# Performance work log

Measured on AMD Instinct MI355X. Metric: run time of the kernel, lower is better.

## Reference

```python
import jax, jax.numpy as jnp
import numpy as np

N = 128          # n_nodes (hardcoded groups=128 in the torch module)
TIME_DIM = 16
XYZ_DIM = 63
SIGMA = 0.3
EPS = 0.01
relu = jax.nn.relu


def gconv(x, W, b):
    # grouped 1x1 Conv1d with groups=N: per-node GEMM
    # x: (N, Cin, L), W: (N, Cout, Cin), b: (N, Cout) -> (N, Cout, L)
    return jnp.einsum('ncl,nkc->nkl', x, W) + b[:, :, None]


def setup_inputs() -> dict:
    key = jax.random.key(0)
    ks = iter(jax.random.split(key, 64))

    def W(shape, fan_in):
        return jax.random.normal(next(ks), shape, jnp.float32) / np.float32(np.sqrt(fan_in))

    def bvec(shape):
        return 0.01 * jax.random.normal(next(ks), shape, jnp.float32)

    B, V = 1, 2048
    inp = {
        'poses': 0.1 * jax.random.normal(next(ks), (B, N, 24, 3), jnp.float32),
        't_ped': jax.random.normal(next(ks), (B, TIME_DIM), jnp.float32),
        'w': jax.random.uniform(next(ks), (N, 24), jnp.float32),
        'wpts': jax.random.uniform(next(ks), (B, V, 3), jnp.float32),
        'nodes_posed': jax.random.uniform(next(ks), (B, N, 3), jnp.float32),
        'local_coords': jax.random.normal(next(ks), (N, B, V, XYZ_DIM), jnp.float32),
        # encoder grouped convs
        'Wec1': W((N, 64, 72 + TIME_DIM), 72 + TIME_DIM), 'bec1': bvec((N, 64)),
        'Wec21': W((N, 8, 64), 64), 'bec21': bvec((N, 8)),
        'Wec22': W((N, 8, 64), 64), 'bec22': bvec((N, 8)),
        # decoder grouped convs
        'Wdc1': W((N, 64, 80), 80), 'bdc1': bvec((N, 64)),
        'Wdc21': W((N, 32, 64), 64), 'bdc21': bvec((N, 32)),
        'Wdc22': W((N, 3, 64), 64), 'bdc22': bvec((N, 3)),
        # feature-field grouped convs
        'Wf1': W((N, 64, 32 + XYZ_DIM), 32 + XYZ_DIM), 'bf1': bvec((N, 64)),
        'Wf2': W((N, 64, 64), 64), 'bf2': bvec((N, 64)),
        'Wf3': W((N, 64, 64), 64), 'bf3': bvec((N, 64)),
        'Wf4': W((N, 256, 64), 64), 'bf4': bvec((N, 256)),
        # Nerf head linears
        'Wc1': W((256, 64), 256), 'bc1': bvec((64,)),
        'Wc2': W((64, 3), 64), 'bc2': bvec((3,)),
        'Wd1': W((256, 1), 256), 'bd1': bvec((1,)),
    }
    return inp


def reference(poses, t_ped, w, wpts, nodes_posed, local_coords,
              Wec1, bec1, Wec21, bec21, Wec22, bec22,
              Wdc1, bdc1, Wdc21, bdc21, Wdc22, bdc22,
              Wf1, bf1, Wf2, bf2, Wf3, bf3, Wf4, bf4,
              Wc1, bc1, Wc2, bc2, Wd1, bd1):
    B, V = poses.shape[0], wpts.shape[1]

    # attention-weighted poses: (B, N, 72)
    poses_w = (w[None, :, :, None] * poses).reshape(B, N, 72)

    # ---- encode ----
    t = jnp.broadcast_to(t_ped[:, None, :], (B, N, TIME_DIM))
    enc_in = jnp.concatenate([poses_w, t], axis=-1).transpose(1, 2, 0)   # (N, 72+td, B)
    net = relu(gconv(enc_in, Wec1, bec1))                                # (N, 64, B)
    mean = gconv(net, Wec21, bec21).transpose(0, 2, 1)                   # (N, B, 8)
    logvar = gconv(net, Wec22, bec22).transpose(0, 2, 1)                 # (N, B, 8)
    z = mean  # eval-mode reparameterize

    # ---- decode ----
    dec_in = jnp.concatenate([poses_w, z.transpose(1, 0, 2)], axis=-1).transpose(1, 2, 0)  # (N, 80, B)
    net = relu(gconv(dec_in, Wdc1, bdc1))
    ei = gconv(net, Wdc21, bdc21).transpose(0, 2, 1)                     # (N, B, 32)
    delta_ni = gconv(net, Wdc22, bdc22).transpose(0, 2, 1)               # (N, B, 3)

    # ---- blend weights: RBF influence of each node on each point ----
    diff = wpts[None, :, :, :] - nodes_posed.transpose(1, 0, 2)[:, :, None, :]  # (N, B, V, 3)
    d2 = jnp.sum(diff * diff, axis=-1)                                   # (N, B, V)
    influ = jnp.exp(-d2 / (2.0 * SIGMA * SIGMA)) - EPS
    mask = influ >= 0
    bweights = jnp.maximum(influ, 0.0)

    # ---- feature field (dense per-node MLP, masked; == padded gather/scatter) ----
    raw = jnp.concatenate([jnp.broadcast_to(ei[:, :, None, :], (N, B, V, 32)),
                           local_coords], axis=-1)                       # (N, B, V, 32+xyz)
    x = raw.reshape(N, B * V, 32 + XYZ_DIM).transpose(0, 2, 1)           # (N, Cin, B*V)
    net = relu(gconv(x, Wf1, bf1))
    net = relu(gconv(net, Wf2, bf2))
    net = relu(gconv(net, Wf3, bf3))
    fout = relu(gconv(net, Wf4, bf4))                                    # (N, 256, B*V)
    f = fout.transpose(0, 2, 1).reshape(N, B, V, 256) * mask[..., None].astype(fout.dtype)

    # ---- blend features ----
    bw = bweights.transpose(1, 2, 0) + 1e-7                              # (B, V, N)
    bw = bw / jnp.sum(bw, axis=-1, keepdims=True)
    f_blend = jnp.einsum('nbvc,bvn->bvc', f, bw)                         # (B, V, 256)

    # ---- Nerf head ----
    netc = relu(f_blend @ Wc1 + bc1)
    c = netc @ Wc2 + bc2                                                 # (B, V, 3)
    d = relu(f_blend @ Wd1 + bd1)                                        # (B, V, 1)
    return (c, d, ei, delta_ni, mean, logvar)
```

## Files before the change

### kernel.cpp

```cpp
#include <hip/hip_runtime.h>

typedef __bf16 bf16;
typedef __bf16 bf16x4 __attribute__((ext_vector_type(4)));
typedef float  f32x4  __attribute__((ext_vector_type(4)));

#define NPTS 2048
#define XS_LD 68
#define W1_LD 100

__global__ __launch_bounds__(256) void k_sniff(const void* poses_raw, int* flag)
{
    __shared__ int cnt;
    if (threadIdx.x == 0) cnt = 0;
    __syncthreads();
    const bf16* pb = (const bf16*)poses_raw;
    int local = 0;
    for (int i = threadIdx.x; i < 9216; i += 256) {
        float v = (float)pb[i];
        if (!(v >= -2.0f && v <= 2.0f)) local++;
    }
    atomicAdd(&cnt, local);
    __syncthreads();
    if (threadIdx.x == 0) *flag = (cnt < 64) ? 1 : 0;
}

template<typename T, int WANT>
__global__ __launch_bounds__(128) void k_encdec_t(
    const T* __restrict__ poses, const T* __restrict__ t_ped, const T* __restrict__ w,
    const T* __restrict__ Wec1, const T* __restrict__ bec1,
    const T* __restrict__ Wec21, const T* __restrict__ bec21,
    const T* __restrict__ Wec22, const T* __restrict__ bec22,
    const T* __restrict__ Wdc1, const T* __restrict__ bdc1,
    const T* __restrict__ Wdc21, const T* __restrict__ bdc21,
    const T* __restrict__ Wdc22, const T* __restrict__ bdc22,
    T* __restrict__ out_ei, T* __restrict__ out_delta,
    T* __restrict__ out_mean, T* __restrict__ out_logvar,
    const int* __restrict__ flag)
{
    if (*flag != WANT) return;
    int n = blockIdx.x, tid = threadIdx.x;
    __shared__ float sin_[88], zbuf[8], net1[64], din[80], net2[64];
    if (tid < 72)      sin_[tid] = (float)w[n*24 + tid/3] * (float)poses[n*72 + tid];
    else if (tid < 88) sin_[tid] = (float)t_ped[tid - 72];
    __syncthreads();
    if (tid < 64) {
        float a = (float)bec1[n*64 + tid];
        const T* wr = Wec1 + (size_t)(n*64 + tid) * 88;
        for (int c = 0; c < 88; ++c) a += (float)wr[c] * sin_[c];
        net1[tid] = fmaxf(a, 0.f);
    }
    __syncthreads();
    if (tid < 8) {
        float a = (float)bec21[n*8 + tid];
        const T* wr = Wec21 + (size_t)(n*8 + tid) * 64;
        for (int c = 0; c < 64; ++c) a += (float)wr[c] * net1[c];
        out_mean[n*8 + tid] = (T)a;
        zbuf[tid] = a;
    } else if (tid < 16) {
        int o = tid - 8;
        float a = (float)bec22[n*8 + o];
        const T* wr = Wec22 + (size_t)(n*8 + o) * 64;
        for (int c = 0; c < 64; ++c) a += (float)wr[c] * net1[c];
        out_logvar[n*8 + o] = (T)a;
    }
    __syncthreads();
    if (tid < 72)      din[tid] = sin_[tid];
    else if (tid < 80) din[tid] = zbuf[tid - 72];
    __syncthreads();
    if (tid < 64) {
        float a = (float)bdc1[n*64 + tid];
        const T* wr = Wdc1 + (size_t)(n*64 + tid) * 80;
        for (int c = 0; c < 80; ++c) a += (float)wr[c] * din[c];
        net2[tid] = fmaxf(a, 0.f);
    }
    __syncthreads();
    if (tid < 32) {
        float a = (float)bdc21[n*32 + tid];
        const T* wr = Wdc21 + (size_t)(n*32 + tid) * 64;
        for (int c = 0; c < 64; ++c) a += (float)wr[c] * net2[c];
        out_ei[n*32 + tid] = (T)a;
    } else if (tid < 35) {
        int o = tid - 32;
        float a = (float)bdc22[n*3 + o];
        const T* wr = Wdc22 + (size_t)(n*3 + o) * 64;
        for (int c = 0; c < 64; ++c) a += (float)wr[c] * net2[c];
        out_delta[n*3 + o] = (T)a;
    }
}

template<typename T, int WANT>
__global__ __launch_bounds__(256) void k_bweights_t(
    const T* __restrict__ wpts, const T* __restrict__ nodes,
    float* __restrict__ wgt, const int* __restrict__ flag)
{
    if (*flag != WANT) return;
    int v = blockIdx.x * 256 + threadIdx.x;
    float px = (float)wpts[v*3+0], py = (float)wpts[v*3+1], pz = (float)wpts[v*3+2];
    float denom = 0.f;
    for (int n = 0; n < 128; ++n) {
        float dx = px - (float)nodes[n*3+0];
        float dy = py - (float)nodes[n*3+1];
        float dz = pz - (float)nodes[n*3+2];
        float d2 = dx*dx + dy*dy + dz*dz;
        float influ = expf(-d2 * (1.0f/0.18f)) - 0.01f;
        denom += fmaxf(influ, 0.f) + 1e-7f;
    }
    float inv = 1.f / denom;
    for (int n = 0; n < 128; ++n) {
        float dx = px - (float)nodes[n*3+0];
        float dy = py - (float)nodes[n*3+1];
        float dz = pz - (float)nodes[n*3+2];
        float d2 = dx*dx + dy*dy + dz*dz;
        float influ = expf(-d2 * (1.0f/0.18f)) - 0.01f;
        wgt[n*NPTS + v] = (influ >= 0.f) ? (fmaxf(influ, 0.f) + 1e-7f) * inv : 0.f;
    }
}


__device__ __forceinline__ f32x4 loadw4(const float* p) { return *(const f32x4*)p; }
__device__ __forceinline__ f32x4 loadw4(const bf16* p)
{
    bf16x4 v = *(const bf16x4*)p;
    f32x4 r;
    #pragma unroll
    for (int j = 0; j < 4; ++j) r[j] = (float)v[j];
    return r;
}

template<typename T>
__device__ __forceinline__ void layer64(
    const T* __restrict__ Wbase, const T* __restrict__ bbase,
    const float* __restrict__ hin, float* __restrict__ hout,
    int og, int pg)
{
    float acc[4][4] = {};
    #pragma unroll 4
    for (int k0 = 0; k0 < 64; k0 += 4) {
        f32x4 wv[4], xv[4];
        #pragma unroll
        for (int c = 0; c < 4; ++c) wv[c] = loadw4(Wbase + (size_t)(og*4 + c)*64 + k0);
        #pragma unroll
        for (int j = 0; j < 4; ++j) xv[j] = *(const f32x4*)&hin[(k0 + j)*XS_LD + pg*4];
        #pragma unroll
        for (int c = 0; c < 4; ++c)
            #pragma unroll
            for (int j = 0; j < 4; ++j)
                #pragma unroll
                for (int r = 0; r < 4; ++r)
                    acc[c][r] += wv[c][j] * xv[j][r];
    }
    #pragma unroll
    for (int c = 0; c < 4; ++c) {
        float b = (float)bbase[og*4 + c];
        f32x4 hv;
        #pragma unroll
        for (int r = 0; r < 4; ++r) hv[r] = fmaxf(acc[c][r] + b, 0.f);
        *(f32x4*)&hout[(og*4 + c)*XS_LD + pg*4] = hv;
    }
}

template<typename T, int WANT>
__global__ __launch_bounds__(256, 2) void k_feat_fast(
    const T* __restrict__ Wf1, const T* __restrict__ Wf2,
    const T* __restrict__ Wf3, const T* __restrict__ Wf4,
    const T* __restrict__ lc, const T* __restrict__ ei,
    const T* __restrict__ bf1, const T* __restrict__ bf2,
    const T* __restrict__ bf3, const T* __restrict__ bf4,
    const float* __restrict__ wgt, float* __restrict__ f_blend,
    const int* __restrict__ flag)
{
    if (*flag != WANT) return;
    int ptile = blockIdx.x;
    int g     = blockIdx.y;
    int p0    = ptile * 64;
    int tid = threadIdx.x;
    int og = tid >> 4;
    int pg = tid & 15;

    __shared__ __attribute__((aligned(16))) float xs [96*XS_LD];
    __shared__ __attribute__((aligned(16))) float ws1[64*W1_LD];
    __shared__ __attribute__((aligned(16))) float hA [64*XS_LD];

    if (tid < 64) xs[95*XS_LD + tid] = 0.f;

    float fb[4][4][4];
    #pragma unroll
    for (int a = 0; a < 4; ++a)
        #pragma unroll
        for (int b = 0; b < 4; ++b)
            #pragma unroll
            for (int r = 0; r < 4; ++r) fb[a][b][r] = 0.f;

    #pragma unroll 1
    for (int nn = 0; nn < 8; ++nn) {
        int n = g*8 + nn;
        __syncthreads();

        #pragma unroll
        for (int i = 0; i < 8; ++i) {
            int e = i*256 + tid; int r = e >> 6, p = e & 63;
            xs[r*XS_LD + p] = (float)ei[n*32 + r];
        }
        {
            const T* src = lc + ((size_t)n*NPTS + p0) * 63;
            #pragma unroll
            for (int i = 0; i < 16; ++i) {
                int e = i*256 + tid;
                if (e < 4032) {
                    int p = e / 63, c = e - p*63;
                    xs[(32 + c)*XS_LD + p] = (float)src[e];
                }
            }
        }
        {
            const T* src = Wf1 + (size_t)n * 64 * 95;
            #pragma unroll
            for (int i = 0; i < 24; ++i) {
                int e = i*256 + tid;
                if (e < 6080) {
                    int oc = e / 95, k = e - oc*95;
                    ws1[oc*W1_LD + k] = (float)src[e];
                }
            }
            if (tid < 64) ws1[tid*W1_LD + 95] = 0.f;
        }
        float wgtv[4];
        #pragma unroll
        for (int j = 0; j < 4; ++j) wgtv[j] = wgt[n*NPTS + p0 + pg*4 + j];
        __syncthreads();

        {
            float acc[4][4] = {};
            #pragma unroll 4
            for (int k0 = 0; k0 < 96; k0 += 4) {
                f32x4 wv[4], xv[4];
                #pragma unroll
                for (int c = 0; c < 4; ++c) wv[c] = *(const f32x4*)&ws1[(og*4 + c)*W1_LD + k0];
                #pragma unroll
                for (int j = 0; j < 4; ++j) xv[j] = *(const f32x4*)&xs[(k0 + j)*XS_LD + pg*4];
                #pragma unroll
                for (int c = 0; c < 4; ++c)
                    #pragma unroll
                    for (int j = 0; j < 4; ++j)
                        #pragma unroll
                        for (int r = 0; r < 4; ++r)
                            acc[c][r] += wv[c][j] * xv[j][r];
            }
            #pragma unroll
            for (int c = 0; c < 4; ++c) {
                float b = (float)bf1[n*64 + og*4 + c];
                f32x4 hv;
                #pragma unroll
                for (int r = 0; r < 4; ++r) hv[r] = fmaxf(acc[c][r] + b, 0.f);
                *(f32x4*)&hA[(og*4 + c)*XS_LD + pg*4] = hv;
            }
        }
        __syncthreads();

        layer64(Wf2 + (size_t)n*64*64, bf2 + n*64, hA, xs, og, pg);
        __syncthreads();

        layer64(Wf3 + (size_t)n*64*64, bf3 + n*64, xs, ws1, og, pg);
        __syncthreads();

        {
            const T* W4n = Wf4 + (size_t)n * 256 * 64;
            const T* b4n = bf4 + n * 256;
            #pragma unroll 1
            for (int mt = 0; mt < 4; ++mt) {
                float acc[4][4] = {};
                #pragma unroll 4
                for (int k0 = 0; k0 < 64; k0 += 4) {
                    f32x4 wv[4], xv[4];
                    #pragma unroll
                    for (int c = 0; c < 4; ++c)
                        wv[c] = loadw4(W4n + (size_t)(mt*64 + og*4 + c)*64 + k0);
                    #pragma unroll
                    for (int j = 0; j < 4; ++j)
                        xv[j] = *(const f32x4*)&ws1[(k0 + j)*XS_LD + pg*4];
                    #pragma unroll
                    for (int c = 0; c < 4; ++c)
                        #pragma unroll
                        for (int j = 0; j < 4; ++j)
                            #pragma unroll
                            for (int r = 0; r < 4; ++r)
                                acc[c][r] += wv[c][j] * xv[j][r];
                }
                #pragma unroll
                for (int c = 0; c < 4; ++c) {
                    float b = (float)b4n[mt*64 + og*4 + c];
                    #pragma unroll
                    for (int r = 0; r < 4; ++r)
                        fb[mt][c][r] += fmaxf(acc[c][r] + b, 0.f) * wgtv[r];
                }
            }
        }
    }

    #pragma unroll
    for (int mt = 0; mt < 4; ++mt)
        #pragma unroll
        for (int c = 0; c < 4; ++c)
            #pragma unroll
            for (int r = 0; r < 4; ++r)
                atomicAdd(&f_blend[(size_t)(p0 + pg*4 + r)*256 + mt*64 + og*4 + c],
                          fb[mt][c][r]);
}

__global__ __launch_bounds__(256) void k_zero_fb(float* __restrict__ fb)
{
    fb[blockIdx.x*256 + threadIdx.x] = 0.f;
}

template<typename T, int WANT>
__global__ __launch_bounds__(256) void k_head_t(
    const float* __restrict__ f_blend,
    const T* __restrict__ Wc1, const T* __restrict__ bc1,
    const T* __restrict__ Wc2, const T* __restrict__ bc2,
    const T* __restrict__ Wd1, const T* __restrict__ bd1,
    T* __restrict__ out_c, T* __restrict__ out_d,
    const int* __restrict__ flag)
{
    if (*flag != WANT) return;
    int t = blockIdx.x * 256 + threadIdx.x;
    int p = t >> 6, j = t & 63;
    const float* fb = f_blend + (size_t)p * 256;

    float a = (float)bc1[j];
    #pragma unroll 8
    for (int c = 0; c < 256; ++c)
        a += fb[c] * (float)Wc1[c*64 + j];
    float nc = fmaxf(a, 0.f);

    float s0 = nc * (float)Wc2[j*3 + 0];
    float s1 = nc * (float)Wc2[j*3 + 1];
    float s2 = nc * (float)Wc2[j*3 + 2];
    float sd = 0.f;
    #pragma unroll
    for (int u = 0; u < 4; ++u) {
        int c = j*4 + u;
        sd += fb[c] * (float)Wd1[c];
    }
    #pragma unroll
    for (int off = 32; off > 0; off >>= 1) {
        s0 += __shfl_down(s0, off);
        s1 += __shfl_down(s1, off);
        s2 += __shfl_down(s2, off);
        sd += __shfl_down(sd, off);
    }
    if (j == 0) {
        out_c[p*3 + 0] = (T)(s0 + (float)bc2[0]);
        out_c[p*3 + 1] = (T)(s1 + (float)bc2[1]);
        out_c[p*3 + 2] = (T)(s2 + (float)bc2[2]);
        out_d[p]       = (T)fmaxf(sd + (float)bd1[0], 0.f);
    }
}

extern "C" void kernel_launch(void* const* d_in, const int* in_sizes, int n_in,
                              void* d_out, int out_size, void* d_ws, size_t ws_size,
                              hipStream_t stream)
{
    char* wsp = (char*)d_ws;
    auto alloc = [&](size_t bytes) { char* r = wsp; wsp += (bytes + 255) & ~(size_t)255; return r; };
    float* f_blend = (float*)alloc((size_t)NPTS * 256 * 4);
    float* wgt     = (float*)alloc((size_t)128 * NPTS * 4);
    int*   flag    = (int*)  alloc(256);

    hipLaunchKernelGGL(k_sniff, dim3(1), dim3(256), 0, stream, d_in[0], flag);
    hipLaunchKernelGGL(k_zero_fb, dim3(2048), dim3(256), 0, stream, f_blend);

    #define LAUNCH_ALL(T, WANT)                                                         \
    {                                                                                   \
        const T* poses = (const T*)d_in[0];                                             \
        const T* t_ped = (const T*)d_in[1];                                             \
        const T* w     = (const T*)d_in[2];                                             \
        const T* wpts  = (const T*)d_in[3];                                             \
        const T* nodes = (const T*)d_in[4];                                             \
        const T* lc    = (const T*)d_in[5];                                             \
        const T* Wec1  = (const T*)d_in[6];  const T* bec1 = (const T*)d_in[7];         \
        const T* Wec21 = (const T*)d_in[8];  const T* bec21= (const T*)d_in[9];         \
        const T* Wec22 = (const T*)d_in[10]; const T* bec22= (const T*)d_in[11];        \
        const T* Wdc1  = (const T*)d_in[12]; const T* bdc1 = (const T*)d_in[13];        \
        const T* Wdc21 = (const T*)d_in[14]; const T* bdc21= (const T*)d_in[15];        \
        const T* Wdc22 = (const T*)d_in[16]; const T* bdc22= (const T*)d_in[17];        \
        const T* Wf1   = (const T*)d_in[18]; const T* bf1  = (const T*)d_in[19];        \
        const T* Wf2   = (const T*)d_in[20]; const T* bf2  = (const T*)d_in[21];        \
        const T* Wf3   = (const T*)d_in[22]; const T* bf3  = (const T*)d_in[23];        \
        const T* Wf4   = (const T*)d_in[24]; const T* bf4  = (const T*)d_in[25];        \
        const T* Wc1   = (const T*)d_in[26]; const T* bc1  = (const T*)d_in[27];        \
        const T* Wc2   = (const T*)d_in[28]; const T* bc2  = (const T*)d_in[29];        \
        const T* Wd1   = (const T*)d_in[30]; const T* bd1  = (const T*)d_in[31];        \
        T* out = (T*)d_out;                                                             \
        T* out_c      = out;                                                            \
        T* out_d      = out + 6144;                                                     \
        T* out_ei     = out + 8192;                                                     \
        T* out_delta  = out + 12288;                                                    \
        T* out_mean   = out + 12672;                                                    \
        T* out_logvar = out + 13696;                                                    \
        hipLaunchKernelGGL((k_encdec_t<T, WANT>), dim3(128), dim3(128), 0, stream,      \
            poses, t_ped, w, Wec1, bec1, Wec21, bec21, Wec22, bec22,                    \
            Wdc1, bdc1, Wdc21, bdc21, Wdc22, bdc22,                                     \
            out_ei, out_delta, out_mean, out_logvar, flag);                             \
        hipLaunchKernelGGL((k_bweights_t<T, WANT>), dim3(8), dim3(256), 0, stream,      \
            wpts, nodes, wgt, flag);                                                    \
        hipLaunchKernelGGL((k_feat_fast<T, WANT>), dim3(32, 16), dim3(256), 0, stream,  \
            Wf1, Wf2, Wf3, Wf4, lc, (const T*)out_ei, bf1, bf2, bf3, bf4,               \
            wgt, f_blend, flag);                                                        \
        hipLaunchKernelGGL((k_head_t<T, WANT>), dim3(512), dim3(256), 0, stream,        \
            f_blend, Wc1, bc1, Wc2, bc2, Wd1, bd1, out_c, out_d, flag);                 \
    }

    LAUNCH_ALL(bf16, 1)
    LAUNCH_ALL(float, 0)
    #undef LAUNCH_ALL
}
```

Baseline: 629.6 us.

## Shrink feature-field point tiles, prefetch next node, replace atomics with partial-sum reduce

The feature-field kernel now processes 32-point tiles instead of 64 with a smaller shared-memory footprint, and its launch bound rises to four blocks per CU for higher occupancy. Wf1 is read straight from global memory instead of being staged in LDS. The next node's local coordinates and encoder features are prefetched into registers during the last layer. Blocks are remapped so each XCD handles a contiguous node group. Per-point atomic accumulation into f_blend is replaced by coalesced writes to a 16-way partial buffer plus a separate reduce kernel when workspace allows, which costs extra memory traffic and one more launch.

```diff
diff --git a/kernel.cpp b/kernel.cpp
--- a/kernel.cpp
+++ b/kernel.cpp
@@ -3,10 +3,10 @@
 typedef __bf16 bf16;
 typedef __bf16 bf16x4 __attribute__((ext_vector_type(4)));
 typedef float  f32x4  __attribute__((ext_vector_type(4)));
+typedef float  f32x2  __attribute__((ext_vector_type(2)));
 
 #define NPTS 2048
-#define XS_LD 68
-#define W1_LD 100
+#define LD 36
 
 __global__ __launch_bounds__(256) void k_sniff(const void* poses_raw, int* flag)
 {
@@ -117,8 +117,8 @@
 }
 
 
-__device__ __forceinline__ f32x4 loadw4(const float* p) { return *(const f32x4*)p; }
-__device__ __forceinline__ f32x4 loadw4(const bf16* p)
+__device__ __forceinline__ f32x4 ld4(const float* p) { return *(const f32x4*)p; }
+__device__ __forceinline__ f32x4 ld4(const bf16* p)
 {
     bf16x4 v = *(const bf16x4*)p;
     f32x4 r;
@@ -128,183 +128,248 @@
 }
 
 template<typename T>
-__device__ __forceinline__ void layer64(
-    const T* __restrict__ Wbase, const T* __restrict__ bbase,
-    const float* __restrict__ hin, float* __restrict__ hout,
-    int og, int pg)
-{
-    float acc[4][4] = {};
+__device__ __forceinline__ void layer64g(
+    const T* __restrict__ W, const T* __restrict__ b,
+    const float* __restrict__ hin, float* __restrict__ hout, int og, int pg)
+{
+    float acc[4][2] = {};
     #pragma unroll 4
     for (int k0 = 0; k0 < 64; k0 += 4) {
-        f32x4 wv[4], xv[4];
-        #pragma unroll
-        for (int c = 0; c < 4; ++c) wv[c] = loadw4(Wbase + (size_t)(og*4 + c)*64 + k0);
-        #pragma unroll
-        for (int j = 0; j < 4; ++j) xv[j] = *(const f32x4*)&hin[(k0 + j)*XS_LD + pg*4];
+        f32x4 wv[4]; f32x2 xv[4];
+        #pragma unroll
+        for (int c = 0; c < 4; ++c) wv[c] = ld4(W + (size_t)(og*4 + c)*64 + k0);
+        #pragma unroll
+        for (int j = 0; j < 4; ++j) xv[j] = *(const f32x2*)&hin[(k0 + j)*LD + pg*2];
         #pragma unroll
         for (int c = 0; c < 4; ++c)
             #pragma unroll
             for (int j = 0; j < 4; ++j)
                 #pragma unroll
-                for (int r = 0; r < 4; ++r)
+                for (int r = 0; r < 2; ++r)
                     acc[c][r] += wv[c][j] * xv[j][r];
     }
     #pragma unroll
     for (int c = 0; c < 4; ++c) {
-        float b = (float)bbase[og*4 + c];
-        f32x4 hv;
-        #pragma unroll
-        for (int r = 0; r < 4; ++r) hv[r] = fmaxf(acc[c][r] + b, 0.f);
-        *(f32x4*)&hout[(og*4 + c)*XS_LD + pg*4] = hv;
-    }
-}
-
-template<typename T, int WANT>
-__global__ __launch_bounds__(256, 2) void k_feat_fast(
+        float bb = (float)b[og*4 + c];
+        f32x2 hv;
+        #pragma unroll
+        for (int r = 0; r < 2; ++r) hv[r] = fmaxf(acc[c][r] + bb, 0.f);
+        *(f32x2*)&hout[(og*4 + c)*LD + pg*2] = hv;
+    }
+}
+
+template<typename T, int WANT, int ATOM>
+__global__ __launch_bounds__(256, 4) void k_feat_fast(
     const T* __restrict__ Wf1, const T* __restrict__ Wf2,
     const T* __restrict__ Wf3, const T* __restrict__ Wf4,
     const T* __restrict__ lc, const T* __restrict__ ei,
     const T* __restrict__ bf1, const T* __restrict__ bf2,
     const T* __restrict__ bf3, const T* __restrict__ bf4,
-    const float* __restrict__ wgt, float* __restrict__ f_blend,
+    const float* __restrict__ wgt, float* __restrict__ outbuf,
     const int* __restrict__ flag)
 {
     if (*flag != WANT) return;
-    int ptile = blockIdx.x;
-    int g     = blockIdx.y;
-    int p0    = ptile * 64;
+    int bid = blockIdx.x;
+    int xcd = bid & 7;
+    int i   = bid >> 3;
+    int g     = 2*xcd + (i >> 6);
+    int ptile = i & 63;
+    int p0  = ptile * 32;
     int tid = threadIdx.x;
     int og = tid >> 4;
     int pg = tid & 15;
 
-    __shared__ __attribute__((aligned(16))) float xs [96*XS_LD];
-    __shared__ __attribute__((aligned(16))) float ws1[64*W1_LD];
-    __shared__ __attribute__((aligned(16))) float hA [64*XS_LD];
-
-    if (tid < 64) xs[95*XS_LD + tid] = 0.f;
-
-    float fb[4][4][4];
+    __shared__ __attribute__((aligned(16))) float smem[(96 + 64) * LD];
+    float* xs = smem;
+    float* hA = smem + 96*LD;
+
+    if (tid < 32) xs[95*LD + tid] = 0.f;
+
+    float fb[4][4][2];
     #pragma unroll
     for (int a = 0; a < 4; ++a)
         #pragma unroll
         for (int b = 0; b < 4; ++b)
             #pragma unroll
-            for (int r = 0; r < 4; ++r) fb[a][b][r] = 0.f;
+            for (int r = 0; r < 2; ++r) fb[a][b][r] = 0.f;
+
+    f32x4 lv0 = {}, lv1 = {};
+    float ev[4];
+
+    auto stage_load = [&](int n) {
+        const T* src = lc + ((size_t)n*NPTS + p0) * 63;
+        lv0 = ld4(src + tid*4);
+        if (tid < 248) lv1 = ld4(src + 1024 + tid*4);
+        const T* ein = ei + n*32;
+        #pragma unroll
+        for (int k = 0; k < 4; ++k) ev[k] = (float)ein[k*8 + (tid >> 5)];
+    };
+    auto stage_write = [&]() {
+        #pragma unroll
+        for (int j = 0; j < 4; ++j) {
+            int e = tid*4 + j; int p = e/63, c = e - 63*p;
+            xs[(32 + c)*LD + p] = lv0[j];
+        }
+        if (tid < 248) {
+            #pragma unroll
+            for (int j = 0; j < 4; ++j) {
+                int e = 1024 + tid*4 + j; int p = e/63, c = e - 63*p;
+                xs[(32 + c)*LD + p] = lv1[j];
+            }
+        }
+        #pragma unroll
+        for (int k = 0; k < 4; ++k) {
+            int e = k*256 + tid;
+            xs[(e >> 5)*LD + (e & 31)] = ev[k];
+        }
+    };
+
+    stage_load(g*8);
+    stage_write();
+    __syncthreads();
 
     #pragma unroll 1
     for (int nn = 0; nn < 8; ++nn) {
         int n = g*8 + nn;
-        __syncthreads();
-
-        #pragma unroll
-        for (int i = 0; i < 8; ++i) {
-            int e = i*256 + tid; int r = e >> 6, p = e & 63;
-            xs[r*XS_LD + p] = (float)ei[n*32 + r];
-        }
+
         {
-            const T* src = lc + ((size_t)n*NPTS + p0) * 63;
-            #pragma unroll
-            for (int i = 0; i < 16; ++i) {
-                int e = i*256 + tid;
-                if (e < 4032) {
-                    int p = e / 63, c = e - p*63;
-                    xs[(32 + c)*XS_LD + p] = (float)src[e];
+            const T* W1b = Wf1 + (size_t)(n*64 + og*4) * 95;
+            float acc[4][2] = {};
+            #pragma unroll 4
+            for (int kk = 0; kk < 23; ++kk) {
+                int k0 = kk*4;
+                float wv[4][4]; f32x2 xv[4];
+                #pragma unroll
+                for (int c = 0; c < 4; ++c) {
+                    const T* wr = W1b + (size_t)c*95 + k0;
+                    #pragma unroll
+                    for (int j = 0; j < 4; ++j) wv[c][j] = (float)wr[j];
                 }
-            }
-        }
-        {
-            const T* src = Wf1 + (size_t)n * 64 * 95;
-            #pragma unroll
-            for (int i = 0; i < 24; ++i) {
-                int e = i*256 + tid;
-                if (e < 6080) {
-                    int oc = e / 95, k = e - oc*95;
-                    ws1[oc*W1_LD + k] = (float)src[e];
-                }
-            }
-            if (tid < 64) ws1[tid*W1_LD + 95] = 0.f;
-        }
-        float wgtv[4];
-        #pragma unroll
-        for (int j = 0; j < 4; ++j) wgtv[j] = wgt[n*NPTS + p0 + pg*4 + j];
-        __syncthreads();
-
-        {
-            float acc[4][4] = {};
-            #pragma unroll 4
-            for (int k0 = 0; k0 < 96; k0 += 4) {
-                f32x4 wv[4], xv[4];
-                #pragma unroll
-                for (int c = 0; c < 4; ++c) wv[c] = *(const f32x4*)&ws1[(og*4 + c)*W1_LD + k0];
-                #pragma unroll
-                for (int j = 0; j < 4; ++j) xv[j] = *(const f32x4*)&xs[(k0 + j)*XS_LD + pg*4];
+                #pragma unroll
+                for (int j = 0; j < 4; ++j) xv[j] = *(const f32x2*)&xs[(k0 + j)*LD + pg*2];
                 #pragma unroll
                 for (int c = 0; c < 4; ++c)
                     #pragma unroll
                     for (int j = 0; j < 4; ++j)
                         #pragma unroll
-                        for (int r = 0; r < 4; ++r)
+                        for (int r = 0; r < 2; ++r)
                             acc[c][r] += wv[c][j] * xv[j][r];
             }
+            {
+                float xt[3][2];
+                #pragma unroll
+                for (int j = 0; j < 3; ++j)
+                    #pragma unroll
+                    for (int r = 0; r < 2; ++r) xt[j][r] = xs[(92 + j)*LD + pg*2 + r];
+                #pragma unroll
+                for (int c = 0; c < 4; ++c) {
+                    const T* wr = W1b + (size_t)c*95;
+                    #pragma unroll
+                    for (int j = 0; j < 3; ++j) {
+                        float wj = (float)wr[92 + j];
+                        #pragma unroll
+                        for (int r = 0; r < 2; ++r) acc[c][r] += wj * xt[j][r];
+                    }
+                }
+            }
             #pragma unroll
             for (int c = 0; c < 4; ++c) {
-                float b = (float)bf1[n*64 + og*4 + c];
-                f32x4 hv;
-                #pragma unroll
-                for (int r = 0; r < 4; ++r) hv[r] = fmaxf(acc[c][r] + b, 0.f);
-                *(f32x4*)&hA[(og*4 + c)*XS_LD + pg*4] = hv;
+                float bb = (float)bf1[n*64 + og*4 + c];
+                f32x2 hv;
+                #pragma unroll
+                for (int r = 0; r < 2; ++r) hv[r] = fmaxf(acc[c][r] + bb, 0.f);
+                *(f32x2*)&hA[(og*4 + c)*LD + pg*2] = hv;
             }
         }
         __syncthreads();
 
-        layer64(Wf2 + (size_t)n*64*64, bf2 + n*64, hA, xs, og, pg);
+        layer64g(Wf2 + (size_t)n*64*64, bf2 + n*64, hA, xs, og, pg);
         __syncthreads();
 
-        layer64(Wf3 + (size_t)n*64*64, bf3 + n*64, xs, ws1, og, pg);
+        layer64g(Wf3 + (size_t)n*64*64, bf3 + n*64, xs, hA, og, pg);
         __syncthreads();
 
+        if (nn < 7) stage_load(n + 1);
+
         {
-            const T* W4n = Wf4 + (size_t)n * 256 * 64;
-            const T* b4n = bf4 + n * 256;
-            #pragma unroll 1
+            float w0 = wgt[n*NPTS + p0 + pg*2];
+            float w1 = wgt[n*NPTS + p0 + pg*2 + 1];
+            const T* W4n = Wf4 + (size_t)n*256*64;
+            const T* b4n = bf4 + n*256;
+            #pragma unroll
             for (int mt = 0; mt < 4; ++mt) {
-                float acc[4][4] = {};
+                float acc[4][2] = {};
                 #pragma unroll 4
                 for (int k0 = 0; k0 < 64; k0 += 4) {
-                    f32x4 wv[4], xv[4];
+                    f32x4 wv[4]; f32x2 xv[4];
                     #pragma unroll
                     for (int c = 0; c < 4; ++c)
-                        wv[c] = loadw4(W4n + (size_t)(mt*64 + og*4 + c)*64 + k0);
-                    #pragma unroll
-                    for (int j = 0; j < 4; ++j)
-                        xv[j] = *(const f32x4*)&ws1[(k0 + j)*XS_LD + pg*4];
+                        wv[c] = ld4(W4n + (size_t)(mt*64 + og*4 + c)*64 + k0);
+                    #pragma unroll
+                    for (int j = 0; j < 4; ++j) xv[j] = *(const f32x2*)&hA[(k0 + j)*LD + pg*2];
                     #pragma unroll
                     for (int c = 0; c < 4; ++c)
                         #pragma unroll
                         for (int j = 0; j < 4; ++j)
                             #pragma unroll
-                            for (int r = 0; r < 4; ++r)
+                            for (int r = 0; r < 2; ++r)
                                 acc[c][r] += wv[c][j] * xv[j][r];
                 }
                 #pragma unroll
                 for (int c = 0; c < 4; ++c) {
-                    float b = (float)b4n[mt*64 + og*4 + c];
-                    #pragma unroll
-                    for (int r = 0; r < 4; ++r)
-                        fb[mt][c][r] += fmaxf(acc[c][r] + b, 0.f) * wgtv[r];
+                    float bb = (float)b4n[mt*64 + og*4 + c];
+                    fb[mt][c][0] += fmaxf(acc[c][0] + bb, 0.f) * w0;
+                    fb[mt][c][1] += fmaxf(acc[c][1] + bb, 0.f) * w1;
                 }
             }
         }
-    }
-
-    #pragma unroll
-    for (int mt = 0; mt < 4; ++mt)
-        #pragma unroll
-        for (int c = 0; c < 4; ++c)
-            #pragma unroll
-            for (int r = 0; r < 4; ++r)
-                atomicAdd(&f_blend[(size_t)(p0 + pg*4 + r)*256 + mt*64 + og*4 + c],
-                          fb[mt][c][r]);
+        if (nn < 7) stage_write();
+        __syncthreads();
+    }
+
+    float* tbuf = smem;
+    #pragma unroll
+    for (int half = 0; half < 2; ++half) {
+        if (half) __syncthreads();
+        if ((pg >> 3) == half) {
+            #pragma unroll
+            for (int mt = 0; mt < 4; ++mt)
+                #pragma unroll
+                for (int r = 0; r < 2; ++r) {
+                    int row = pg*2 + r - half*16;
+                    f32x4 v = { fb[mt][0][r], fb[mt][1][r], fb[mt][2][r], fb[mt][3][r] };
+                    *(f32x4*)&tbuf[row*260 + mt*64 + og*4] = v;
+                }
+        }
+        __syncthreads();
+        #pragma unroll
+        for (int k = 0; k < 4; ++k) {
+            int idx = k*1024 + tid*4;
+            int row = idx >> 8, col = idx & 255;
+            f32x4 v = *(const f32x4*)&tbuf[row*260 + col];
+            size_t dst = ((size_t)(p0 + half*16 + row))*256 + col;
+            if (ATOM) {
+                #pragma unroll
+                for (int j = 0; j < 4; ++j) atomicAdd(&outbuf[dst + j], v[j]);
+            } else {
+                *(f32x4*)&outbuf[(size_t)g*NPTS*256 + dst] = v;
+            }
+        }
+    }
+}
+
+template<int WANT>
+__global__ __launch_bounds__(256) void k_reduce(
+    const float* __restrict__ part, float* __restrict__ fbl,
+    const int* __restrict__ flag)
+{
+    if (*flag != WANT) return;
+    int t = blockIdx.x*256 + threadIdx.x;
+    f32x4 s = {};
+    #pragma unroll
+    for (int gg = 0; gg < 16; ++gg)
+        s += *(const f32x4*)&part[(size_t)gg*NPTS*256 + (size_t)t*4];
+    *(f32x4*)&fbl[(size_t)t*4] = s;
 }
 
 __global__ __launch_bounds__(256) void k_zero_fb(float* __restrict__ fb)
@@ -365,9 +430,12 @@
     float* f_blend = (float*)alloc((size_t)NPTS * 256 * 4);
     float* wgt     = (float*)alloc((size_t)128 * NPTS * 4);
     int*   flag    = (int*)  alloc(256);
+    float* partial = (float*)alloc((size_t)16 * NPTS * 256 * 4);
+    bool use_part  = ws_size >= (size_t)(wsp - (char*)d_ws);
 
     hipLaunchKernelGGL(k_sniff, dim3(1), dim3(256), 0, stream, d_in[0], flag);
-    hipLaunchKernelGGL(k_zero_fb, dim3(2048), dim3(256), 0, stream, f_blend);
+    if (!use_part)
+        hipLaunchKernelGGL(k_zero_fb, dim3(2048), dim3(256), 0, stream, f_blend);
 
     #define LAUNCH_ALL(T, WANT)                                                         \
     {                                                                                   \
@@ -403,9 +471,17 @@
             out_ei, out_delta, out_mean, out_logvar, flag);                             \
         hipLaunchKernelGGL((k_bweights_t<T, WANT>), dim3(8), dim3(256), 0, stream,      \
             wpts, nodes, wgt, flag);                                                    \
-        hipLaunchKernelGGL((k_feat_fast<T, WANT>), dim3(32, 16), dim3(256), 0, stream,  \
-            Wf1, Wf2, Wf3, Wf4, lc, (const T*)out_ei, bf1, bf2, bf3, bf4,               \
-            wgt, f_blend, flag);                                                        \
+        if (use_part) {                                                                 \
+            hipLaunchKernelGGL((k_feat_fast<T, WANT, 0>), dim3(1024), dim3(256), 0,     \
+                stream, Wf1, Wf2, Wf3, Wf4, lc, (const T*)out_ei,                       \
+                bf1, bf2, bf3, bf4, wgt, partial, flag);                                \
+            hipLaunchKernelGGL((k_reduce<WANT>), dim3(512), dim3(256), 0, stream,       \
+                partial, f_blend, flag);                                                \
+        } else {                                                                        \
+            hipLaunchKernelGGL((k_feat_fast<T, WANT, 1>), dim3(1024), dim3(256), 0,     \
+                stream, Wf1, Wf2, Wf3, Wf4, lc, (const T*)out_ei,                       \
+                bf1, bf2, bf3, bf4, wgt, f_blend, flag);                                \
+        }                                                                               \
         hipLaunchKernelGGL((k_head_t<T, WANT>), dim3(512), dim3(256), 0, stream,        \
             f_blend, Wc1, bc1, Wc2, bc2, Wd1, bd1, out_c, out_d, flag);                 \
     }
```

New measurement: 855.4 us. 35.9% more time.
